# Kernel optimization log

Measured on AMD Instinct MI355X. Metric: run time of the kernel, lower is better.

## Reference

```python
import jax, jax.numpy as jnp
import numpy as np

ANCHOR_LENGTHS = jnp.array([1., 2., 3., 4., 5., 7., 9.], dtype=jnp.float32)  # A = 7


def make_anchors_1d(Lf):
    # anchors [Lf*A, 2] in feature coords, matching torch make_anchors_1d
    centers = jnp.arange(Lf, dtype=jnp.float32) + 0.5          # [Lf]
    c = centers[:, None]                                        # [Lf,1]
    w = ANCHOR_LENGTHS[None, :]                                 # [1,A]
    start = c - 0.5 * w
    end = c + 0.5 * w
    return jnp.stack(jnp.broadcast_arrays(start, end), axis=-1).reshape(-1, 2)


def setup_inputs() -> dict:
    key = jax.random.key(0)
    ks = jax.random.split(key, 4)
    B, C, Lf, A = 8, 512, 16384, 7
    feat = jax.random.normal(ks[0], (B, C, Lf), dtype=jnp.float32)
    conv_w = jax.random.normal(ks[1], (C, C, 3), dtype=jnp.float32) * 0.02
    conv_b = jnp.zeros((C,), dtype=jnp.float32)
    obj_w = jax.random.normal(ks[2], (A, C, 1), dtype=jnp.float32) * 0.02
    obj_b = jnp.zeros((A,), dtype=jnp.float32)
    reg_w = jax.random.normal(ks[3], (A * 2, C, 1), dtype=jnp.float32) * 0.02
    reg_b = jnp.zeros((A * 2,), dtype=jnp.float32)
    return {"feat": feat, "conv_w": conv_w, "conv_b": conv_b,
            "obj_w": obj_w, "obj_b": obj_b, "reg_w": reg_w, "reg_b": reg_b}


def reference(feat, conv_w, conv_b, obj_w, obj_b, reg_w, reg_b):
    B, C, Lf = feat.shape
    A = obj_w.shape[0]
    # conv1d k=3 pad=1 (NCH layout), + bias, relu
    h = jax.lax.conv_general_dilated(
        feat, conv_w, window_strides=(1,), padding=((1, 1),),
        dimension_numbers=("NCH", "OIH", "NCH"))
    h = jax.nn.relu(h + conv_b[None, :, None])                  # [B,C,Lf]
    # 1x1 heads as channel contractions
    obj = jnp.einsum("bcl,ac->bla", h, obj_w[:, :, 0]) + obj_b  # [B,Lf,A]
    reg = jnp.einsum("bcl,oc->blo", h, reg_w[:, :, 0]) + reg_b  # [B,Lf,2A]
    obj = obj.reshape(B, Lf * A)                                # [B,N]
    reg = reg.reshape(B, Lf, A, 2).reshape(B, Lf * A, 2)        # [B,N,2]
    anchors = make_anchors_1d(Lf)                               # [N,2]
    return obj, reg, anchors
```

## Files before the change

kernel.cpp:

```cpp
#include <hip/hip_runtime.h>
#include <hip/hip_bf16.h>
#include <stdint.h>

typedef __attribute__((ext_vector_type(4))) float f32x4;
typedef __attribute__((ext_vector_type(16))) float f32x16;
typedef __attribute__((ext_vector_type(4))) int i32x4;
typedef __attribute__((ext_vector_type(8))) int i32x8;
typedef __attribute__((ext_vector_type(8))) short bh8;
typedef unsigned short u16;
typedef unsigned int u32;
typedef unsigned char u8;

#define B_    8
#define C_    512
#define LF    16384
#define KTOT  1536
#define SCL   0x7F7F7F7Fu

#define P4_BYTES ((size_t)4 * B_ * 21 * LF * 4)
#define W8_OFF   P4_BYTES

#define OBJ_OFF  0
#define REG_OFF  917504
#define ANC_OFF  2752512

__device__ __forceinline__ u32 pk2bf(float lo, float hi) {
    u32 r;
    asm("v_cvt_pk_bf16_f32 %0, %1, %2" : "=v"(r) : "v"(lo), "v"(hi));
    return r;
}
__device__ __forceinline__ void gload16(const u8* g, u8* l) {
    __builtin_amdgcn_global_load_lds(
        (const __attribute__((address_space(1))) void*)g,
        (__attribute__((address_space(3))) void*)l, 16, 0, 0);
}

__global__ void k_cast_w(const float* __restrict__ cw, u8* __restrict__ W8) {
    int i = blockIdx.x * 256 + threadIdx.x;
    if (i >= C_ * KTOT / 2) return;
    int co = i / (KTOT / 2);
    int rr = (i % (KTOT / 2)) * 2;
    int t = rr / 512, q = rr % 512;
    int kc = q >> 6, cc = q & 63;
    int jl = (cc >> 4) ^ ((co >> 1) & 3);
    int ci = kc * 64 + jl * 16 + (cc & 15);
    float f0 = cw[(co * C_ + ci) * 3 + t];
    float f1 = cw[(co * C_ + ci + 1) * 3 + t];
    u32 pk = __builtin_amdgcn_cvt_pk_fp8_f32(f0, f1, 0, false);
    *(u16*)&W8[(size_t)co * KTOT + rr] = (u16)pk;
}

__global__ void k_anchors(float* __restrict__ out) {
    int l = blockIdx.x * 256 + threadIdx.x;
    if (l >= LF) return;
    const float AL[7] = {1.f, 2.f, 3.f, 4.f, 5.f, 7.f, 9.f};
    float c = (float)l + 0.5f;
    float* an = out + ANC_OFF + (size_t)l * 14;
#pragma unroll
    for (int a = 0; a < 7; ++a) {
        an[a * 2 + 0] = c - 0.5f * AL[a];
        an[a * 2 + 1] = c + 0.5f * AL[a];
    }
}

__global__ __launch_bounds__(256, 4) void k_conv_head(
    const float* __restrict__ feat, const u8* __restrict__ W8,
    const float* __restrict__ conv_b, const float* __restrict__ obj_w,
    const float* __restrict__ reg_w, float* __restrict__ P4) {
    __shared__ __align__(16) char smem[33024];
    u8* As3 = (u8*)smem;
    u8* Bs  = (u8*)(smem + 24576);
    u16* Hs = (u16*)smem;
    u16* Wp = (u16*)(smem + 16384);

    const int tid = threadIdx.x;
    const int lane = tid & 63, wave = tid >> 6;
    const int wm = wave >> 1, wn = wave & 1;
    const int g = lane >> 4, cL = lane & 15;
    const int r32 = lane & 31, hK = lane >> 5;

    const int wg = (blockIdx.x & 7) * 512 + (blockIdx.x >> 3);
    const int mt = wg & 3;
    const int l0 = ((wg >> 2) & 127) * 128;
    const int b  = wg >> 9;
    const int co0 = mt * 128;

    const int cg = tid & 15, lgrp = tid >> 4;

    f32x16 acc[2][2];
#pragma unroll
    for (int mi = 0; mi < 2; ++mi)
#pragma unroll
        for (int ni = 0; ni < 2; ++ni)
#pragma unroll
            for (int r = 0; r < 16; ++r) acc[mi][ni][r] = 0.f;

    for (int kc = 0; kc < 8; ++kc) {
        __syncthreads();
#pragma unroll
        for (int t = 0; t < 3; ++t)
#pragma unroll
            for (int p = 0; p < 2; ++p) {
                const int row = p * 64 + (tid >> 2);
                const int colB = (tid & 3) * 16;
                gload16(&W8[(size_t)(co0 + row) * KTOT + t * 512 + kc * 64 + colB],
                        &As3[t * 8192 + row * 64 + colB]);
            }
        {
            const float* fp = feat +
                ((size_t)(b * C_ + kc * 64 + cg * 4)) * LF + l0 + lgrp * 8;
            const int slog = cg >> 2;
            const int soff = (cg * 4) & 15;
#pragma unroll
            for (int h = 0; h < 2; ++h) {
                float4 v0 = *(const float4*)(fp + 0 * LF + h * 4);
                float4 v1 = *(const float4*)(fp + 1 * LF + h * 4);
                float4 v2 = *(const float4*)(fp + 2 * LF + h * 4);
                float4 v3 = *(const float4*)(fp + 3 * LF + h * 4);
#pragma unroll
                for (int e = 0; e < 4; ++e) {
                    const int r = 1 + lgrp * 8 + h * 4 + e;
                    u32 w0 = __builtin_amdgcn_cvt_pk_fp8_f32(
                        ((const float*)&v0)[e], ((const float*)&v1)[e], 0, false);
                    u32 w  = __builtin_amdgcn_cvt_pk_fp8_f32(
                        ((const float*)&v2)[e], ((const float*)&v3)[e], w0, true);
                    const int pc = ((slog ^ ((r >> 1) & 3)) * 16) + soff;
                    *(u32*)&Bs[r * 64 + pc] = w;
                }
            }
        }
        if (tid < 128) {
            const int ci2 = tid >> 1;
            const int rr = (tid & 1) ? 129 : 0;
            const int l = l0 + ((tid & 1) ? 128 : -1);
            float v = (l >= 0 && l < LF)
                          ? feat[((size_t)(b * C_ + kc * 64 + ci2)) * LF + l]
                          : 0.f;
            u32 p = __builtin_amdgcn_cvt_pk_fp8_f32(v, 0.f, 0, false);
            const int pc = (((ci2 >> 4) ^ ((rr >> 1) & 3)) * 16) + (ci2 & 15);
            Bs[rr * 64 + pc] = (u8)p;
        }
        __syncthreads();
#pragma unroll
        for (int t = 0; t < 3; ++t) {
            const u8* At = As3 + t * 8192;
            i32x8 af[2], bf[2];
#pragma unroll
            for (int mi = 0; mi < 2; ++mi) {
                const int row = wm * 64 + mi * 32 + r32;
                const int x = (row >> 1) & 3;
                i32x4 a0 = *(const i32x4*)&At[row * 64 + (((2 * hK) ^ x) * 16)];
                i32x4 a1 = *(const i32x4*)&At[row * 64 + (((2 * hK + 1) ^ x) * 16)];
                af[mi] = __builtin_shufflevector(a0, a1, 0, 1, 2, 3, 4, 5, 6, 7);
            }
#pragma unroll
            for (int ni = 0; ni < 2; ++ni) {
                const int row = wn * 64 + ni * 32 + r32 + t;
                const int x = (row >> 1) & 3;
                i32x4 b0 = *(const i32x4*)&Bs[row * 64 + (((2 * hK) ^ x) * 16)];
                i32x4 b1 = *(const i32x4*)&Bs[row * 64 + (((2 * hK + 1) ^ x) * 16)];
                bf[ni] = __builtin_shufflevector(b0, b1, 0, 1, 2, 3, 4, 5, 6, 7);
            }
#pragma unroll
            for (int mi = 0; mi < 2; ++mi)
#pragma unroll
                for (int ni = 0; ni < 2; ++ni)
                    acc[mi][ni] = __builtin_amdgcn_mfma_scale_f32_32x32x64_f8f6f4(
                        af[mi], bf[ni], acc[mi][ni], 0, 0, 0, SCL, 0, SCL);
        }
    }
    __syncthreads();

#pragma unroll
    for (int it = 0; it < 4; ++it) {
        const int q = it * 256 + tid;
        const int a = q >> 5, c0 = (q & 31) * 4;
        float4 wv = {0.f, 0.f, 0.f, 0.f};
        if (a < 7)       wv = *(const float4*)&obj_w[a * C_ + co0 + c0];
        else if (a < 21) wv = *(const float4*)&reg_w[(a - 7) * C_ + co0 + c0];
        uint2 pk;
        pk.x = pk2bf(wv.x, wv.y);
        pk.y = pk2bf(wv.z, wv.w);
        *(uint2*)&Wp[a * 128 + (c0 ^ ((a & 7) << 3))] = pk;
    }

    float* P4base = P4 + ((size_t)(mt * B_ + b) * 21) * LF + l0;
#pragma unroll
    for (int half = 0; half < 2; ++half) {
        if (wn == half) {
#pragma unroll
            for (int mi = 0; mi < 2; ++mi)
#pragma unroll
                for (int ni = 0; ni < 2; ++ni) {
                    const int l_half = ni * 32 + r32;
                    const int xw = (l_half & 7) << 3;
#pragma unroll
                    for (int q = 0; q < 4; ++q) {
                        const int cb = wm * 64 + mi * 32 + q * 8 + 4 * hK;
                        const float b0_ = conv_b[co0 + cb + 0];
                        const float b1_ = conv_b[co0 + cb + 1];
                        const float b2_ = conv_b[co0 + cb + 2];
                        const float b3_ = conv_b[co0 + cb + 3];
                        uint2 pk;
                        pk.x = pk2bf(fmaxf(acc[mi][ni][q * 4 + 0] + b0_, 0.f),
                                     fmaxf(acc[mi][ni][q * 4 + 1] + b1_, 0.f));
                        pk.y = pk2bf(fmaxf(acc[mi][ni][q * 4 + 2] + b2_, 0.f),
                                     fmaxf(acc[mi][ni][q * 4 + 3] + b3_, 0.f));
                        *(uint2*)&Hs[l_half * 128 + (cb ^ xw)] = pk;
                    }
                }
        }
        __syncthreads();

        f32x4 hacc0 = {0.f, 0.f, 0.f, 0.f};
        f32x4 hacc1 = {0.f, 0.f, 0.f, 0.f};
        const int lrow = wave * 16 + cL;
        const int swA = (cL & 7) << 3;
#pragma unroll
        for (int ks2 = 0; ks2 < 4; ++ks2) {
            const int ko = ks2 * 32 + g * 8;
            bh8 wa0 = *(const bh8*)&Wp[cL * 128 + (ko ^ swA)];
            bh8 wa1 = *(const bh8*)&Wp[(16 + cL) * 128 + (ko ^ swA)];
            bh8 hb  = *(const bh8*)&Hs[lrow * 128 + (ko ^ swA)];
            hacc0 = __builtin_amdgcn_mfma_f32_16x16x32_bf16(wa0, hb, hacc0, 0, 0, 0);
            hacc1 = __builtin_amdgcn_mfma_f32_16x16x32_bf16(wa1, hb, hacc1, 0, 0, 0);
        }
        const int lg = half * 64 + lrow;
#pragma unroll
        for (int m = 0; m < 2; ++m) {
            const int a0 = m * 16 + g * 4;
            const f32x4 hv = (m == 0) ? hacc0 : hacc1;
#pragma unroll
            for (int r = 0; r < 4; ++r) {
                const int a = a0 + r;
                if (a < 21) P4base[(size_t)a * LF + lg] = hv[r];
            }
        }
        __syncthreads();
    }
}

__global__ void k_finalize(const float* __restrict__ P4, const float* __restrict__ obj_b,
                           const float* __restrict__ reg_b, float* __restrict__ out) {
    int gid = blockIdx.x * 256 + threadIdx.x;
    if (gid >= B_ * LF) return;
    int b = gid >> 14, l = gid & (LF - 1);
    float s[21];
#pragma unroll
    for (int a = 0; a < 21; ++a) {
        float v = 0.f;
#pragma unroll
        for (int m = 0; m < 4; ++m) v += P4[((size_t)(m * B_ + b) * 21 + a) * LF + l];
        s[a] = v;
    }
    float* op = out + OBJ_OFF + (size_t)b * (LF * 7) + (size_t)l * 7;
#pragma unroll
    for (int a = 0; a < 7; ++a) op[a] = s[a] + obj_b[a];
    float* rp = out + REG_OFF + (size_t)b * (LF * 14) + (size_t)l * 14;
#pragma unroll
    for (int o = 0; o < 14; ++o) rp[o] = s[7 + o] + reg_b[o];
}

extern "C" void kernel_launch(void* const* d_in, const int* in_sizes, int n_in,
                              void* d_out, int out_size, void* d_ws, size_t ws_size,
                              hipStream_t stream) {
    const float* feat   = (const float*)d_in[0];
    const float* conv_w = (const float*)d_in[1];
    const float* conv_b = (const float*)d_in[2];
    const float* obj_w  = (const float*)d_in[3];
    const float* obj_b  = (const float*)d_in[4];
    const float* reg_w  = (const float*)d_in[5];
    const float* reg_b  = (const float*)d_in[6];
    char* ws = (char*)d_ws;
    float* P4 = (float*)ws;
    u8* W8    = (u8*)(ws + W8_OFF);
    float* out = (float*)d_out;

    k_cast_w<<<1536, 256, 0, stream>>>(conv_w, W8);
    k_anchors<<<64, 256, 0, stream>>>(out);
    k_conv_head<<<4096, 256, 0, stream>>>(feat, W8, conv_b, obj_w, reg_w, P4);
    k_finalize<<<(B_ * LF + 255) / 256, 256, 0, stream>>>(P4, obj_b, reg_b, out);
}
```

Before: 225.9 us.

## Pre-transpose features to swizzled fp8 buffer and stream via global_load_lds

Adds a pre-pass that transposes feat into a channel-fastest, pre-swizzled fp8 workspace with zero halo rows. The main conv kernel then copies its B tile with direct global-to-LDS loads instead of strided fp32 loads, in-register conversion and scattered LDS stores. Each feature element is now converted once rather than once per output-channel tile (4x). The cost is an extra kernel that reads all of feat and writes an fp8 copy, plus an additional launch.

```diff
diff --git a/kernel.cpp b/kernel.cpp
--- a/kernel.cpp
+++ b/kernel.cpp
@@ -15,10 +15,14 @@
 #define C_    512
 #define LF    16384
 #define KTOT  1536
+#define FTR   (LF + 2)
 #define SCL   0x7F7F7F7Fu
 
-#define P4_BYTES ((size_t)4 * B_ * 21 * LF * 4)
-#define W8_OFF   P4_BYTES
+#define P4_BYTES  ((size_t)4 * B_ * 21 * LF * 4)
+#define W8_OFF    P4_BYTES
+#define W8_BYTES  ((size_t)C_ * KTOT)
+#define FT8_OFF   (W8_OFF + W8_BYTES)
+#define FT8_BYTES ((size_t)B_ * 8 * FTR * 64)
 
 #define OBJ_OFF  0
 #define REG_OFF  917504
@@ -50,6 +54,48 @@
     *(u16*)&W8[(size_t)co * KTOT + rr] = (u16)pk;
 }
 
+__global__ __launch_bounds__(256) void k_transpose8(const float* __restrict__ feat,
+                                                    u8* __restrict__ FT8) {
+    __shared__ float Tt[64][65];
+    const int b = blockIdx.z, kc = blockIdx.y, l0t = blockIdx.x * 64;
+    const int tid = threadIdx.x;
+    const int ciL = tid >> 2, lq = (tid & 3) * 16;
+    const float* fp = feat + ((size_t)(b * C_ + kc * 64 + ciL)) * LF + l0t + lq;
+#pragma unroll
+    for (int it = 0; it < 4; ++it) {
+        float4 v = *(const float4*)(fp + it * 4);
+        Tt[lq + it * 4 + 0][ciL] = v.x;
+        Tt[lq + it * 4 + 1][ciL] = v.y;
+        Tt[lq + it * 4 + 2][ciL] = v.z;
+        Tt[lq + it * 4 + 3][ciL] = v.w;
+    }
+    __syncthreads();
+    const int l = tid >> 2, sp = tid & 3;
+    const int lg = l0t + l;
+    const int x = ((((lg & 127) + 1) >> 1) & 3);
+    const int sl = sp ^ x;
+    u32 w[4];
+#pragma unroll
+    for (int j = 0; j < 4; ++j) {
+        float a0 = Tt[l][sl * 16 + j * 4 + 0];
+        float a1 = Tt[l][sl * 16 + j * 4 + 1];
+        float a2 = Tt[l][sl * 16 + j * 4 + 2];
+        float a3 = Tt[l][sl * 16 + j * 4 + 3];
+        u32 t0 = __builtin_amdgcn_cvt_pk_fp8_f32(a0, a1, 0, false);
+        w[j] = __builtin_amdgcn_cvt_pk_fp8_f32(a2, a3, t0, true);
+    }
+    uint4 o; o.x = w[0]; o.y = w[1]; o.z = w[2]; o.w = w[3];
+    *(uint4*)&FT8[(((size_t)(b * 8 + kc)) * FTR + lg + 1) * 64 + sp * 16] = o;
+}
+
+__global__ void k_zero_pad8(u8* __restrict__ FT8) {
+    int i = blockIdx.x * 256 + threadIdx.x;
+    if (i >= 2048) return;
+    int p = i >> 5, j = i & 31;
+    size_t row = (j < 16) ? 0 : (size_t)(LF + 1);
+    *(u32*)&FT8[((size_t)p * FTR + row) * 64 + (j & 15) * 4] = 0;
+}
+
 __global__ void k_anchors(float* __restrict__ out) {
     int l = blockIdx.x * 256 + threadIdx.x;
     if (l >= LF) return;
@@ -64,7 +110,7 @@
 }
 
 __global__ __launch_bounds__(256, 4) void k_conv_head(
-    const float* __restrict__ feat, const u8* __restrict__ W8,
+    const u8* __restrict__ FT8, const u8* __restrict__ W8,
     const float* __restrict__ conv_b, const float* __restrict__ obj_w,
     const float* __restrict__ reg_w, float* __restrict__ P4) {
     __shared__ __align__(16) char smem[33024];
@@ -85,8 +131,6 @@
     const int b  = wg >> 9;
     const int co0 = mt * 128;
 
-    const int cg = tid & 15, lgrp = tid >> 4;
-
     f32x16 acc[2][2];
 #pragma unroll
     for (int mi = 0; mi < 2; ++mi)
@@ -107,38 +151,12 @@
                         &As3[t * 8192 + row * 64 + colB]);
             }
         {
-            const float* fp = feat +
-                ((size_t)(b * C_ + kc * 64 + cg * 4)) * LF + l0 + lgrp * 8;
-            const int slog = cg >> 2;
-            const int soff = (cg * 4) & 15;
-#pragma unroll
-            for (int h = 0; h < 2; ++h) {
-                float4 v0 = *(const float4*)(fp + 0 * LF + h * 4);
-                float4 v1 = *(const float4*)(fp + 1 * LF + h * 4);
-                float4 v2 = *(const float4*)(fp + 2 * LF + h * 4);
-                float4 v3 = *(const float4*)(fp + 3 * LF + h * 4);
-#pragma unroll
-                for (int e = 0; e < 4; ++e) {
-                    const int r = 1 + lgrp * 8 + h * 4 + e;
-                    u32 w0 = __builtin_amdgcn_cvt_pk_fp8_f32(
-                        ((const float*)&v0)[e], ((const float*)&v1)[e], 0, false);
-                    u32 w  = __builtin_amdgcn_cvt_pk_fp8_f32(
-                        ((const float*)&v2)[e], ((const float*)&v3)[e], w0, true);
-                    const int pc = ((slog ^ ((r >> 1) & 3)) * 16) + soff;
-                    *(u32*)&Bs[r * 64 + pc] = w;
-                }
-            }
-        }
-        if (tid < 128) {
-            const int ci2 = tid >> 1;
-            const int rr = (tid & 1) ? 129 : 0;
-            const int l = l0 + ((tid & 1) ? 128 : -1);
-            float v = (l >= 0 && l < LF)
-                          ? feat[((size_t)(b * C_ + kc * 64 + ci2)) * LF + l]
-                          : 0.f;
-            u32 p = __builtin_amdgcn_cvt_pk_fp8_f32(v, 0.f, 0, false);
-            const int pc = (((ci2 >> 4) ^ ((rr >> 1) & 3)) * 16) + (ci2 & 15);
-            Bs[rr * 64 + pc] = (u8)p;
+            const u8* bsrc = FT8 + (((size_t)(b * 8 + kc)) * FTR + l0) * 64;
+#pragma unroll
+            for (int q2 = 0; q2 < 2; ++q2)
+                gload16(bsrc + (q2 * 256 + tid) * 16, Bs + (q2 * 256 + tid) * 16);
+            if (tid < 8)
+                gload16(bsrc + (512 + tid) * 16, Bs + (512 + tid) * 16);
         }
         __syncthreads();
 #pragma unroll
@@ -225,7 +243,7 @@
             hacc0 = __builtin_amdgcn_mfma_f32_16x16x32_bf16(wa0, hb, hacc0, 0, 0, 0);
             hacc1 = __builtin_amdgcn_mfma_f32_16x16x32_bf16(wa1, hb, hacc1, 0, 0, 0);
         }
-        const int lg = half * 64 + lrow;
+        const int lg2 = half * 64 + lrow;
 #pragma unroll
         for (int m = 0; m < 2; ++m) {
             const int a0 = m * 16 + g * 4;
@@ -233,7 +251,7 @@
 #pragma unroll
             for (int r = 0; r < 4; ++r) {
                 const int a = a0 + r;
-                if (a < 21) P4base[(size_t)a * LF + lg] = hv[r];
+                if (a < 21) P4base[(size_t)a * LF + lg2] = hv[r];
             }
         }
         __syncthreads();
@@ -274,10 +292,14 @@
     char* ws = (char*)d_ws;
     float* P4 = (float*)ws;
     u8* W8    = (u8*)(ws + W8_OFF);
+    u8* FT8   = (u8*)(ws + FT8_OFF);
     float* out = (float*)d_out;
 
     k_cast_w<<<1536, 256, 0, stream>>>(conv_w, W8);
+    k_zero_pad8<<<8, 256, 0, stream>>>(FT8);
+    dim3 gt(LF / 64, 8, B_);
+    k_transpose8<<<gt, 256, 0, stream>>>(feat, FT8);
     k_anchors<<<64, 256, 0, stream>>>(out);
-    k_conv_head<<<4096, 256, 0, stream>>>(feat, W8, conv_b, obj_w, reg_w, P4);
+    k_conv_head<<<4096, 256, 0, stream>>>(FT8, W8, conv_b, obj_w, reg_w, P4);
     k_finalize<<<(B_ * LF + 255) / 256, 256, 0, stream>>>(P4, obj_b, reg_b, out);
 }
```

New measurement: 559.2 us. 148% more time.
